# Kernel optimization log

Measured on AMD Instinct MI355X. Metric: run time of the kernel, lower is better.

Reference implementation:

```python
import jax, jax.numpy as jnp
import numpy as np

N_HEADS = 16
ROPE = 64        # qk_rope_head_dim
KV_LORA = 512
V_DIM = 128
THETA = 10000.0

def rms_norm(x, w, eps=1e-6):
    return x * jax.lax.rsqrt(jnp.mean(x * x, axis=-1, keepdims=True) + eps) * w

def rope_cos_sin(T, d, theta=THETA):
    half = d // 2
    inv = 1.0 / theta ** (jnp.arange(half, dtype=jnp.float32) / half)
    ang = jnp.arange(T, dtype=jnp.float32)[:, None] * inv  # (T, half)
    return jnp.cos(ang), jnp.sin(ang)

def apply_rot(x, cos, sin):
    # x: (B,T,H,D); complex rotation on interleaved pairs
    xr, xi = x[..., 0::2], x[..., 1::2]
    c = cos[None, :, None, :]
    s = sin[None, :, None, :]
    orr = xr * c - xi * s
    oi = xr * s + xi * c
    return jnp.stack([orr, oi], axis=-1).reshape(x.shape)

def setup_inputs() -> dict:
    key = jax.random.key(0)
    ks = jax.random.split(key, 8)
    B, T, C = 2, 2048, 2048
    QLR = 1536
    x = jax.random.normal(ks[0], (B, T, C), dtype=jnp.float32)
    mask = jnp.tril(jnp.ones((T, T), dtype=jnp.int32))[None, None]
    sc = 0.02
    w_qa = jax.random.normal(ks[1], (QLR, C), dtype=jnp.float32) * sc
    qa_norm_w = jnp.ones((QLR,), dtype=jnp.float32)
    w_qb = jax.random.normal(ks[2], (N_HEADS * 2 * ROPE, QLR), dtype=jnp.float32) * sc
    w_kva = jax.random.normal(ks[3], (KV_LORA + ROPE, C), dtype=jnp.float32) * sc
    kva_norm_w = jnp.ones((KV_LORA,), dtype=jnp.float32)
    w_kvb = jax.random.normal(ks[4], (N_HEADS * (ROPE + V_DIM), KV_LORA), dtype=jnp.float32) * sc
    w_o = jax.random.normal(ks[5], (C, N_HEADS * V_DIM), dtype=jnp.float32) * sc
    return {"x": x, "mask": mask, "w_qa": w_qa, "qa_norm_w": qa_norm_w, "w_qb": w_qb,
            "w_kva": w_kva, "kva_norm_w": kva_norm_w, "w_kvb": w_kvb, "w_o": w_o}

def reference(x, mask, w_qa, qa_norm_w, w_qb, w_kva, kva_norm_w, w_kvb, w_o):
    B, T, C = x.shape
    # Q: low-rank compress -> norm -> up-project, split nope/rope halves
    q_c = rms_norm(x @ w_qa.T, qa_norm_w)
    q = (q_c @ w_qb.T).reshape(B, T, N_HEADS, 2 * ROPE)
    q_nope, q_rope = q[..., :ROPE], q[..., ROPE:]
    # KV: joint low-rank + shared rope key
    kv_a = x @ w_kva.T
    kv_c = rms_norm(kv_a[..., :KV_LORA], kva_norm_w)
    k_rope_raw = kv_a[..., KV_LORA:]                       # (B,T,ROPE)
    kv = (kv_c @ w_kvb.T).reshape(B, T, N_HEADS, ROPE + V_DIM)
    k_content, v = kv[..., :ROPE], kv[..., ROPE:]
    k_rope = jnp.broadcast_to(k_rope_raw[:, :, None, :], (B, T, N_HEADS, ROPE))
    cos, sin = rope_cos_sin(T, ROPE)
    q_rope = apply_rot(q_rope, cos, sin)
    k_rope = apply_rot(k_rope, cos, sin)
    q = jnp.concatenate([q_nope, q_rope], axis=-1)         # (B,T,H,2*ROPE)
    k = jnp.concatenate([k_content, k_rope], axis=-1)
    att = jnp.einsum('bqhd,bkhd->bhqk', q, k) * (ROPE ** -0.5)
    att = jnp.where(mask == 0, -jnp.inf, att)
    att = jax.nn.softmax(att, axis=-1)
    # source's nan-guard: uniform attention if any nan appeared
    att = jnp.where(jnp.any(jnp.isnan(att)), jnp.float32(1.0 / T), att)
    out = jnp.einsum('bhqk,bkhd->bqhd', att, v).reshape(B, T, N_HEADS * V_DIM)
    return out @ w_o.T
```

## Files before the change

### kernel.cpp

```cpp
#include <hip/hip_runtime.h>

typedef short bf16x8 __attribute__((ext_vector_type(8)));
typedef unsigned short u16x8 __attribute__((ext_vector_type(8)));
typedef unsigned short u16x4 __attribute__((ext_vector_type(4)));
typedef float f32x4 __attribute__((ext_vector_type(4)));
typedef unsigned u32x4 __attribute__((ext_vector_type(4)));
typedef unsigned u32x2 __attribute__((ext_vector_type(2)));

#define DEV static __device__ __forceinline__

DEV float bf2f(unsigned short u) { return __uint_as_float(((unsigned)u) << 16); }
DEV unsigned short f2bf(float f) {
  unsigned u = __float_as_uint(f);
  return (unsigned short)((u + 0x7fffu + ((u >> 16) & 1u)) >> 16);
}
DEV unsigned cvtpk(float lo, float hi) {
  unsigned r;
  asm("v_cvt_pk_bf16_f32 %0, %1, %2" : "=v"(r) : "v"(lo), "v"(hi));
  return r;
}
DEV void p32swap(unsigned& a, unsigned& b) {
  asm volatile("v_permlane32_swap_b32 %0, %1" : "+v"(a), "+v"(b));
}
DEV void p16swap(unsigned& a, unsigned& b) {
  asm volatile("v_permlane16_swap_b32 %0, %1" : "+v"(a), "+v"(b));
}

#define GLDS16(g, l)                                                                   \
  __builtin_amdgcn_global_load_lds((const __attribute__((address_space(1))) void*)(g), \
                                   (__attribute__((address_space(3))) void*)(l), 16, 0, 0)

DEV void cvt_body(const float* __restrict__ src, unsigned short* __restrict__ dst,
                  int rows, int cols, int dstRows, int bid) {
  int i = bid * 256 + (int)threadIdx.x;
  int e = i << 2;
  int r = e / cols;
  int c = e - r * cols;
  u16x4 o = {0, 0, 0, 0};
  if (r < rows) {
    const float* p = src + (size_t)r * cols + c;
    o[0] = f2bf(p[0]); o[1] = f2bf(p[1]); o[2] = f2bf(p[2]); o[3] = f2bf(p[3]);
  }
  *(u16x4*)(dst + e) = o;
}

__global__ __launch_bounds__(256) void convert_all(
    const float* __restrict__ x, const float* __restrict__ w_qa, const float* __restrict__ w_kva,
    const float* __restrict__ w_qb, const float* __restrict__ w_kvb, const float* __restrict__ w_o,
    unsigned short* __restrict__ xb, unsigned short* __restrict__ wqkva,
    unsigned short* __restrict__ wqbb, unsigned short* __restrict__ wkvbb,
    unsigned short* __restrict__ wob) {
  int bid = blockIdx.x;
  if (bid < 8192)        cvt_body(x,     xb,                        4096, 2048, 4096, bid);
  else if (bid < 11264)  cvt_body(w_qa,  wqkva,                     1536, 2048, 1536, bid - 8192);
  else if (bid < 12544)  cvt_body(w_kva, wqkva + (size_t)1536*2048,  576, 2048,  640, bid - 11264);
  else if (bid < 15616)  cvt_body(w_qb,  wqbb,                      2048, 1536, 2048, bid - 12544);
  else if (bid < 17152)  cvt_body(w_kvb, wkvbb,                     3072,  512, 3072, bid - 15616);
  else                   cvt_body(w_o,   wob,                       2048, 2048, 2048, bid - 17152);
}

template <typename OutT>
__global__ __launch_bounds__(256, 2) void gemm_bt(const unsigned short* __restrict__ A,
                                                  const unsigned short* __restrict__ B,
                                                  OutT* __restrict__ C, int M, int N, int K) {
  __shared__ __align__(16) unsigned short As[128 * 64];
  __shared__ __align__(16) unsigned short Bs[128 * 64];
  const int tid = threadIdx.x;
  const int lane = tid & 63, wave = tid >> 6;
  const int l16 = lane & 15, lhi = lane >> 4;
  const int nbn = N >> 7;
  const int bm = blockIdx.x / nbn, bn = blockIdx.x - bm * nbn;
  const int m0 = bm << 7, n0 = bn << 7;
  const int wm = (wave >> 1) << 6, wn = (wave & 1) << 6;
  f32x4 acc[4][4] = {};
  for (int k0 = 0; k0 < K; k0 += 64) {
#pragma unroll
    for (int it = 0; it < 4; ++it) {
      int slot = it * 256 + tid;
      int row = slot >> 3, col = (slot & 7) << 3;
      GLDS16(A + (size_t)(m0 + row) * K + k0 + col, As + (it * 256 + wave * 64) * 8);
      GLDS16(B + (size_t)(n0 + row) * K + k0 + col, Bs + (it * 256 + wave * 64) * 8);
    }
    __syncthreads();
#pragma unroll
    for (int ks = 0; ks < 2; ++ks) {
      bf16x8 a[4], b[4];
#pragma unroll
      for (int i = 0; i < 4; ++i) {
        a[i] = *(const bf16x8*)(As + (wm + i * 16 + l16) * 64 + ks * 32 + lhi * 8);
        b[i] = *(const bf16x8*)(Bs + (wn + i * 16 + l16) * 64 + ks * 32 + lhi * 8);
      }
#pragma unroll
      for (int i = 0; i < 4; ++i)
#pragma unroll
        for (int j = 0; j < 4; ++j)
          acc[i][j] = __builtin_amdgcn_mfma_f32_16x16x32_bf16(a[i], b[j], acc[i][j], 0, 0, 0);
    }
    __syncthreads();
  }
#pragma unroll
  for (int i = 0; i < 4; ++i)
#pragma unroll
    for (int j = 0; j < 4; ++j)
#pragma unroll
      for (int r = 0; r < 4; ++r) {
        int row = m0 + wm + i * 16 + lhi * 4 + r;
        int col = n0 + wn + j * 16 + l16;
        float v = acc[i][j][r];
        if constexpr (sizeof(OutT) == 4)
          C[(size_t)row * N + col] = v;
        else
          C[(size_t)row * N + col] = (OutT)f2bf(v);
      }
}

__global__ __launch_bounds__(256, 2) void gemm_kvb(const unsigned short* __restrict__ A,
                                                   const unsigned short* __restrict__ B,
                                                   unsigned short* __restrict__ kvfull,
                                                   unsigned short* __restrict__ VT) {
  const int M = 4096, N = 3072, K = 512;
  __shared__ __align__(16) unsigned short As[128 * 64];
  __shared__ __align__(16) unsigned short Bs[128 * 64];
  const int tid = threadIdx.x;
  const int lane = tid & 63, wave = tid >> 6;
  const int l16 = lane & 15, lhi = lane >> 4;
  const int nbn = N >> 7;
  const int bm = blockIdx.x / nbn, bn = blockIdx.x - bm * nbn;
  const int m0 = bm << 7, n0 = bn << 7;
  const int wm = (wave >> 1) << 6, wn = (wave & 1) << 6;
  f32x4 acc[4][4] = {};
  for (int k0 = 0; k0 < K; k0 += 64) {
#pragma unroll
    for (int it = 0; it < 4; ++it) {
      int slot = it * 256 + tid;
      int row = slot >> 3, col = (slot & 7) << 3;
      GLDS16(A + (size_t)(m0 + row) * K + k0 + col, As + (it * 256 + wave * 64) * 8);
      GLDS16(B + (size_t)(n0 + row) * K + k0 + col, Bs + (it * 256 + wave * 64) * 8);
    }
    __syncthreads();
#pragma unroll
    for (int ks = 0; ks < 2; ++ks) {
      bf16x8 a[4], b[4];
#pragma unroll
      for (int i = 0; i < 4; ++i) {
        a[i] = *(const bf16x8*)(As + (wm + i * 16 + l16) * 64 + ks * 32 + lhi * 8);
        b[i] = *(const bf16x8*)(Bs + (wn + i * 16 + l16) * 64 + ks * 32 + lhi * 8);
      }
#pragma unroll
      for (int i = 0; i < 4; ++i)
#pragma unroll
        for (int j = 0; j < 4; ++j)
          acc[i][j] = __builtin_amdgcn_mfma_f32_16x16x32_bf16(a[i], b[j], acc[i][j], 0, 0, 0);
    }
    __syncthreads();
  }
#pragma unroll
  for (int i = 0; i < 4; ++i)
#pragma unroll
    for (int j = 0; j < 4; ++j) {
      int col = n0 + wn + j * 16 + l16;
      int h = col / 192;
      int jc = col - h * 192;
      int row0 = m0 + wm + i * 16 + lhi * 4;
      if (jc < 64) {
#pragma unroll
        for (int r = 0; r < 4; ++r)
          kvfull[(size_t)(row0 + r) * 3072 + col] = f2bf(acc[i][j][r]);
      } else {
        int d = jc - 64;
        int b = row0 >> 11, t0 = row0 & 2047;
        u16x4 pk;
#pragma unroll
        for (int r = 0; r < 4; ++r) pk[r] = f2bf(acc[i][j][r]);
        *(u16x4*)(VT + ((size_t)((b * 16 + h) * 128 + d)) * 2048 + t0) = pk;
      }
    }
}

__global__ __launch_bounds__(256) void rms_fused(const unsigned short* __restrict__ qkva,
                                                 const float* __restrict__ qw,
                                                 const float* __restrict__ kvw,
                                                 unsigned short* __restrict__ q_c,
                                                 unsigned short* __restrict__ kv_c,
                                                 unsigned short* __restrict__ krope) {
  const int row = blockIdx.x, tid = threadIdx.x;
  const unsigned short* p = qkva + (size_t)row * 2176;
  float fq[8];
  float ssq = 0.f;
  const bool act = tid < 192;
  if (act) {
    u16x8 v = *(const u16x8*)(p + tid * 8);
#pragma unroll
    for (int j = 0; j < 8; ++j) { fq[j] = bf2f(v[j]); ssq += fq[j] * fq[j]; }
  }
  float f0 = bf2f(p[1536 + tid * 2]), f1 = bf2f(p[1536 + tid * 2 + 1]);
  float sskv = f0 * f0 + f1 * f1;
#pragma unroll
  for (int m = 1; m <= 32; m <<= 1) {
    ssq += __shfl_xor(ssq, m);
    sskv += __shfl_xor(sskv, m);
  }
  __shared__ float rq[4], rkv[4];
  if ((tid & 63) == 0) { rq[tid >> 6] = ssq; rkv[tid >> 6] = sskv; }
  __syncthreads();
  float rstdq = rsqrtf((rq[0] + rq[1] + rq[2] + rq[3]) * (1.f / 1536.f) + 1e-6f);
  float rstdkv = rsqrtf((rkv[0] + rkv[1] + rkv[2] + rkv[3]) * (1.f / 512.f) + 1e-6f);
  if (act) {
    u16x8 o;
#pragma unroll
    for (int j = 0; j < 8; ++j) o[j] = f2bf(fq[j] * rstdq * qw[tid * 8 + j]);
    *(u16x8*)(q_c + (size_t)row * 1536 + tid * 8) = o;
  }
  kv_c[(size_t)row * 512 + tid * 2]     = f2bf(f0 * rstdkv * kvw[tid * 2]);
  kv_c[(size_t)row * 512 + tid * 2 + 1] = f2bf(f1 * rstdkv * kvw[tid * 2 + 1]);
  if (tid < 32) {
    int j = tid;
    float xr = bf2f(p[2048 + 2 * j]), xi = bf2f(p[2048 + 2 * j + 1]);
    int t = row & 2047;
    float ang = (float)t * powf(10000.f, -(float)j * (1.f / 32.f));
    float c = cosf(ang), s = sinf(ang);
    krope[(size_t)row * 64 + 2 * j]     = f2bf(xr * c - xi * s);
    krope[(size_t)row * 64 + 2 * j + 1] = f2bf(xr * s + xi * c);
  }
}

__global__ __launch_bounds__(256, 4) void flash_attn(const unsigned short* __restrict__ qfull,
                                                     const unsigned short* __restrict__ kvfull,
                                                     const unsigned short* __restrict__ krope,
                                                     const unsigned short* __restrict__ Vt,
                                                     unsigned short* __restrict__ out) {
  const int tid = threadIdx.x, lane = tid & 63, wave = tid >> 6;
  const int l16 = lane & 15, lhi = lane >> 4;
  const int bid = blockIdx.x;
  const int xcd = bid & 7, Lb = bid >> 3;
  const int bhl = Lb >> 5, cL = Lb & 31;
  const int s = (bhl & 1) ? (31 - cL) : cL;
  const int bh = xcd * 4 + bhl;
  const int h = bh & 15, b = bh >> 4;
  __shared__ __align__(16) unsigned short Ks[64 * 128];
  __shared__ __align__(16) unsigned short Vs[64 * 128];

  const float QSCALE = 0.125f * 1.44269504089f;
  bf16x8 qf[4];
  f32x4 o_acc[8] = {};
  const int qg = s * 64 + wave * 16 + l16;
  {
    const unsigned short* qrow = qfull + (size_t)(b * 2048 + qg) * 2048 + h * 128;
#pragma unroll
    for (int ks = 0; ks < 4; ++ks) {
      u16x8 raw = *(const u16x8*)(qrow + ks * 32 + lhi * 8);
      float f[8];
#pragma unroll
      for (int j = 0; j < 8; ++j) f[j] = bf2f(raw[j]);
      if (ks >= 2) {
#pragma unroll
        for (int pp = 0; pp < 4; ++pp) {
          int d = ks * 32 + lhi * 8 + 2 * pp;
          int jl = (d - 64) >> 1;
          float ang = (float)qg * powf(10000.f, -(float)jl * (1.f / 32.f));
          float co = cosf(ang), si = sinf(ang);
          float xr = f[2 * pp], xi = f[2 * pp + 1];
          f[2 * pp] = xr * co - xi * si;
          f[2 * pp + 1] = xr * si + xi * co;
        }
      }
      bf16x8 fr;
#pragma unroll
      for (int j = 0; j < 8; ++j) fr[j] = (short)f2bf(f[j] * QSCALE);
      qf[ks] = fr;
    }
  }
  float m_run = -1e30f, l_run = 0.f;

  const int bT = b * 2048;
  const unsigned short* Vbh = Vt + (size_t)(b * 16 + h) * 128 * 2048;

  for (int kt = 0; kt <= s; ++kt) {
#pragma unroll
    for (int it = 0; it < 4; ++it) {
      int Lo = it * 4096 + wave * 1024 + lane * 16;
      int r = Lo >> 8;
      int w = (Lo & 255) ^ ((r & 7) << 4);
      int cc = w >> 1;
      int tl = bT + kt * 64 + r;
      const unsigned short* src = (cc < 64) ? kvfull + (size_t)tl * 3072 + h * 192 + cc
                                            : krope + (size_t)tl * 64 + (cc - 64);
      GLDS16(src, Ks + ((it * 4096 + wave * 1024) >> 1));
    }
#pragma unroll
    for (int it = 0; it < 4; ++it) {
      int Lo = it * 4096 + wave * 1024 + lane * 16;
      int d = Lo >> 7;
      int w = (Lo & 127) ^ ((d & 7) << 4);
      GLDS16(Vbh + (size_t)d * 2048 + kt * 64 + (w >> 1), Vs + ((it * 4096 + wave * 1024) >> 1));
    }
    __syncthreads();

    f32x4 st[4] = {};
    __builtin_amdgcn_s_setprio(1);
#pragma unroll
    for (int ks = 0; ks < 4; ++ks) {
      bf16x8 kf;
#pragma unroll
      for (int nt = 0; nt < 4; ++nt) {
        int row = nt * 16 + l16;
        int byteoff = row * 256 + ((ks * 64 + lhi * 16) ^ ((l16 & 7) << 4));
        kf = *(const bf16x8*)((const char*)Ks + byteoff);
        st[nt] = __builtin_amdgcn_mfma_f32_16x16x32_bf16(kf, qf[ks], st[nt], 0, 0, 0);
      }
    }
    __builtin_amdgcn_s_setprio(0);

    if (kt == s) {
#pragma unroll
      for (int nt = 0; nt < 4; ++nt)
#pragma unroll
        for (int r = 0; r < 4; ++r) {
          int kg = kt * 64 + nt * 16 + lhi * 4 + r;
          st[nt][r] = (kg <= qg) ? st[nt][r] : -1e30f;
        }
    }
    float mx = -1e30f;
#pragma unroll
    for (int nt = 0; nt < 4; ++nt)
#pragma unroll
      for (int r = 0; r < 4; ++r) mx = fmaxf(mx, st[nt][r]);
    mx = fmaxf(mx, __shfl_xor(mx, 16));
    mx = fmaxf(mx, __shfl_xor(mx, 32));
    if (__ballot(mx > m_run + 8.f)) {
      float mnew = fmaxf(m_run, mx);
      float sc = exp2f(m_run - mnew);
      m_run = mnew;
      l_run *= sc;
#pragma unroll
      for (int dt = 0; dt < 8; ++dt) o_acc[dt] *= sc;
    }
    const float mcur = m_run;
    float sum = 0.f;
#pragma unroll
    for (int nt = 0; nt < 4; ++nt)
#pragma unroll
      for (int r = 0; r < 4; ++r) {
        float p = exp2f(st[nt][r] - mcur);
        st[nt][r] = p;
        sum += p;
      }
    sum += __shfl_xor(sum, 16);
    sum += __shfl_xor(sum, 32);
    l_run += sum;
    bf16x8 pw[2];
    {
      unsigned pk01[4], pk23[4];
#pragma unroll
      for (int nt = 0; nt < 4; ++nt) {
        pk01[nt] = cvtpk(st[nt][0], st[nt][1]);
        pk23[nt] = cvtpk(st[nt][2], st[nt][3]);
      }
#pragma unroll
      for (int k2 = 0; k2 < 2; ++k2) {
        unsigned a0 = pk01[2 * k2], b0 = pk01[2 * k2 + 1];
        unsigned a1 = pk23[2 * k2], b1 = pk23[2 * k2 + 1];
        p32swap(a0, b0); p16swap(a0, b0);
        p32swap(a1, b1); p16swap(a1, b1);
        u32x4 t4 = {a0, a1, b0, b1};
        pw[k2] = *(bf16x8*)&t4;
      }
    }

    __builtin_amdgcn_s_setprio(1);
#pragma unroll
    for (int k2 = 0; k2 < 2; ++k2)
#pragma unroll
      for (int dt = 0; dt < 8; ++dt) {
        int row = dt * 16 + l16;
        int byteoff = row * 128 + ((k2 * 64 + lhi * 16) ^ ((l16 & 7) << 4));
        bf16x8 vf = *(const bf16x8*)((const char*)Vs + byteoff);
        o_acc[dt] = __builtin_amdgcn_mfma_f32_16x16x32_bf16(vf, pw[k2], o_acc[dt], 0, 0, 0);
      }
    __builtin_amdgcn_s_setprio(0);

    __syncthreads();
  }

  {
    float inv = 1.0f / l_run;
    unsigned short* orow = out + (size_t)(b * 2048 + qg) * 2048 + h * 128;
#pragma unroll
    for (int dt = 0; dt < 8; ++dt) {
      unsigned w01 = cvtpk(o_acc[dt][0] * inv, o_acc[dt][1] * inv);
      unsigned w23 = cvtpk(o_acc[dt][2] * inv, o_acc[dt][3] * inv);
      u32x2 st2 = {w01, w23};
      *(u32x2*)(orow + dt * 16 + lhi * 4) = st2;
    }
  }
}

extern "C" void kernel_launch(void* const* d_in, const int* in_sizes, int n_in,
                              void* d_out, int out_size, void* d_ws, size_t ws_size,
                              hipStream_t stream) {
  (void)in_sizes; (void)n_in; (void)out_size; (void)ws_size;
  const float* x      = (const float*)d_in[0];
  const float* w_qa   = (const float*)d_in[2];
  const float* qa_nw  = (const float*)d_in[3];
  const float* w_qb   = (const float*)d_in[4];
  const float* w_kva  = (const float*)d_in[5];
  const float* kva_nw = (const float*)d_in[6];
  const float* w_kvb  = (const float*)d_in[7];
  const float* w_o    = (const float*)d_in[8];
  float* out = (float*)d_out;
  char* ws = (char*)d_ws;

  unsigned short* xb     = (unsigned short*)(ws + 0);
  unsigned short* wqkva  = (unsigned short*)(ws + 16777216);
  unsigned short* wqbb   = (unsigned short*)(ws + 25690112);
  unsigned short* wkvbb  = (unsigned short*)(ws + 31981568);
  unsigned short* wob    = (unsigned short*)(ws + 35127296);
  unsigned short* qkva   = (unsigned short*)(ws + 43515904);
  unsigned short* qfull  = (unsigned short*)(ws + 43515904);
  unsigned short* q_c    = (unsigned short*)(ws + 61341696);
  unsigned short* kv_c   = (unsigned short*)(ws + 73924608);
  unsigned short* krope  = (unsigned short*)(ws + 78118912);
  unsigned short* attno  = (unsigned short*)(ws + 61341696);
  unsigned short* Vattn  = (unsigned short*)(ws + 78643200);
  unsigned short* kvfull = (unsigned short*)d_out;

  convert_all<<<21248, 256, 0, stream>>>(x, w_qa, w_kva, w_qb, w_kvb, w_o,
                                         xb, wqkva, wqbb, wkvbb, wob);

  gemm_bt<unsigned short><<<32 * 17, 256, 0, stream>>>(xb, wqkva, qkva, 4096, 2176, 2048);

  rms_fused<<<4096, 256, 0, stream>>>(qkva, qa_nw, kva_nw, q_c, kv_c, krope);

  gemm_bt<unsigned short><<<32 * 16, 256, 0, stream>>>(q_c, wqbb, qfull, 4096, 2048, 1536);
  gemm_kvb<<<32 * 24, 256, 0, stream>>>(kv_c, wkvbb, kvfull, Vattn);

  flash_attn<<<1024, 256, 0, stream>>>(qfull, kvfull, krope, Vattn, attno);

  gemm_bt<float><<<32 * 16, 256, 0, stream>>>(attno, wob, out, 4096, 2048, 2048);
}
```

Baseline: 282.0 us.

## Double-buffer K/V tiles and process two query subtiles per wave in flash attention

Each block now handles 128 query rows (each wave owns two 16-row subtiles), so every K/V tile loaded into shared memory feeds twice as many MFMAs. K/V staging is double-buffered so the next tile's global-to-LDS loads overlap compute on the current one. The grid is halved and blocks are ordered longest-first to balance the causal workload. The cost is higher register and LDS use (launch bounds lowered to 2 blocks per SIMD), which reduces occupancy, and waves whose causal range is shorter sit idle on the last tile.

```diff
diff --git a/kernel.cpp b/kernel.cpp
--- a/kernel.cpp
+++ b/kernel.cpp
@@ -224,7 +224,7 @@
   }
 }
 
-__global__ __launch_bounds__(256, 4) void flash_attn(const unsigned short* __restrict__ qfull,
+__global__ __launch_bounds__(256, 2) void flash_attn(const unsigned short* __restrict__ qfull,
                                                      const unsigned short* __restrict__ kvfull,
                                                      const unsigned short* __restrict__ krope,
                                                      const unsigned short* __restrict__ Vt,
@@ -232,20 +232,24 @@
   const int tid = threadIdx.x, lane = tid & 63, wave = tid >> 6;
   const int l16 = lane & 15, lhi = lane >> 4;
   const int bid = blockIdx.x;
-  const int xcd = bid & 7, Lb = bid >> 3;
-  const int bhl = Lb >> 5, cL = Lb & 31;
-  const int s = (bhl & 1) ? (31 - cL) : cL;
+  const int xcd = bid & 7, idx = bid >> 3;
+  const int s = 15 - (idx >> 2);
+  const int bhl = idx & 3;
   const int bh = xcd * 4 + bhl;
   const int h = bh & 15, b = bh >> 4;
-  __shared__ __align__(16) unsigned short Ks[64 * 128];
-  __shared__ __align__(16) unsigned short Vs[64 * 128];
+  __shared__ __align__(16) unsigned short Ks[2][64 * 128];
+  __shared__ __align__(16) unsigned short Vs[2][64 * 128];
 
   const float QSCALE = 0.125f * 1.44269504089f;
-  bf16x8 qf[4];
-  f32x4 o_acc[8] = {};
-  const int qg = s * 64 + wave * 16 + l16;
-  {
-    const unsigned short* qrow = qfull + (size_t)(b * 2048 + qg) * 2048 + h * 128;
+  bf16x8 qf[2][4];
+  float m_run[2], l_run[2];
+  int qg[2];
+  f32x4 o_acc[2][8] = {};
+#pragma unroll
+  for (int u = 0; u < 2; ++u) {
+    const int t = s * 128 + wave * 32 + u * 16 + l16;
+    qg[u] = t;
+    const unsigned short* qrow = qfull + (size_t)(b * 2048 + t) * 2048 + h * 128;
 #pragma unroll
     for (int ks = 0; ks < 4; ++ks) {
       u16x8 raw = *(const u16x8*)(qrow + ks * 32 + lhi * 8);
@@ -257,7 +261,7 @@
         for (int pp = 0; pp < 4; ++pp) {
           int d = ks * 32 + lhi * 8 + 2 * pp;
           int jl = (d - 64) >> 1;
-          float ang = (float)qg * powf(10000.f, -(float)jl * (1.f / 32.f));
+          float ang = (float)t * powf(10000.f, -(float)jl * (1.f / 32.f));
           float co = cosf(ang), si = sinf(ang);
           float xr = f[2 * pp], xi = f[2 * pp + 1];
           f[2 * pp] = xr * co - xi * si;
@@ -267,15 +271,18 @@
       bf16x8 fr;
 #pragma unroll
       for (int j = 0; j < 8; ++j) fr[j] = (short)f2bf(f[j] * QSCALE);
-      qf[ks] = fr;
-    }
-  }
-  float m_run = -1e30f, l_run = 0.f;
+      qf[u][ks] = fr;
+    }
+    m_run[u] = -1e30f;
+    l_run[u] = 0.f;
+  }
 
   const int bT = b * 2048;
   const unsigned short* Vbh = Vt + (size_t)(b * 16 + h) * 128 * 2048;
-
-  for (int kt = 0; kt <= s; ++kt) {
+  const int ntiles = 2 * s + 2;
+  const int ktmax = 2 * s + (wave >> 1);
+
+  auto stageK = [&](int kt, int buf) {
 #pragma unroll
     for (int it = 0; it < 4; ++it) {
       int Lo = it * 4096 + wave * 1024 + lane * 16;
@@ -285,110 +292,132 @@
       int tl = bT + kt * 64 + r;
       const unsigned short* src = (cc < 64) ? kvfull + (size_t)tl * 3072 + h * 192 + cc
                                             : krope + (size_t)tl * 64 + (cc - 64);
-      GLDS16(src, Ks + ((it * 4096 + wave * 1024) >> 1));
-    }
+      GLDS16(src, &Ks[buf][(it * 4096 + wave * 1024) >> 1]);
+    }
+  };
+  auto stageV = [&](int kt, int buf) {
 #pragma unroll
     for (int it = 0; it < 4; ++it) {
       int Lo = it * 4096 + wave * 1024 + lane * 16;
       int d = Lo >> 7;
       int w = (Lo & 127) ^ ((d & 7) << 4);
-      GLDS16(Vbh + (size_t)d * 2048 + kt * 64 + (w >> 1), Vs + ((it * 4096 + wave * 1024) >> 1));
-    }
+      GLDS16(Vbh + (size_t)d * 2048 + kt * 64 + (w >> 1), &Vs[buf][(it * 4096 + wave * 1024) >> 1]);
+    }
+  };
+
+  stageK(0, 0);
+  stageV(0, 0);
+  __syncthreads();
+  int cur = 0;
+
+  for (int kt = 0; kt < ntiles; ++kt) {
+    if (kt + 1 < ntiles) { stageK(kt + 1, cur ^ 1); stageV(kt + 1, cur ^ 1); }
+    if (kt <= ktmax) {
+      const unsigned short* Kb = Ks[cur];
+      const unsigned short* Vb = Vs[cur];
+
+      f32x4 st[2][4] = {};
+      __builtin_amdgcn_s_setprio(1);
+#pragma unroll
+      for (int ks = 0; ks < 4; ++ks) {
+        bf16x8 kf[4];
+#pragma unroll
+        for (int nt = 0; nt < 4; ++nt) {
+          int row = nt * 16 + l16;
+          int byteoff = row * 256 + ((ks * 64 + lhi * 16) ^ ((l16 & 7) << 4));
+          kf[nt] = *(const bf16x8*)((const char*)Kb + byteoff);
+        }
+#pragma unroll
+        for (int nt = 0; nt < 4; ++nt) {
+          st[0][nt] = __builtin_amdgcn_mfma_f32_16x16x32_bf16(kf[nt], qf[0][ks], st[0][nt], 0, 0, 0);
+          st[1][nt] = __builtin_amdgcn_mfma_f32_16x16x32_bf16(kf[nt], qf[1][ks], st[1][nt], 0, 0, 0);
+        }
+      }
+      __builtin_amdgcn_s_setprio(0);
+
+      bf16x8 pw[2][2];
+#pragma unroll
+      for (int u = 0; u < 2; ++u) {
+        if (kt == ktmax) {
+#pragma unroll
+          for (int nt = 0; nt < 4; ++nt)
+#pragma unroll
+            for (int r = 0; r < 4; ++r) {
+              int kg = kt * 64 + nt * 16 + lhi * 4 + r;
+              st[u][nt][r] = (kg <= qg[u]) ? st[u][nt][r] : -1e30f;
+            }
+        }
+        float mx = -1e30f;
+#pragma unroll
+        for (int nt = 0; nt < 4; ++nt)
+#pragma unroll
+          for (int r = 0; r < 4; ++r) mx = fmaxf(mx, st[u][nt][r]);
+        mx = fmaxf(mx, __shfl_xor(mx, 16));
+        mx = fmaxf(mx, __shfl_xor(mx, 32));
+        if (__ballot(mx > m_run[u] + 8.f)) {
+          float mnew = fmaxf(m_run[u], mx);
+          float sc = exp2f(m_run[u] - mnew);
+          m_run[u] = mnew;
+          l_run[u] *= sc;
+#pragma unroll
+          for (int dt = 0; dt < 8; ++dt) o_acc[u][dt] *= sc;
+        }
+        const float mcur = m_run[u];
+        float sum = 0.f;
+#pragma unroll
+        for (int nt = 0; nt < 4; ++nt)
+#pragma unroll
+          for (int r = 0; r < 4; ++r) {
+            float p = exp2f(st[u][nt][r] - mcur);
+            st[u][nt][r] = p;
+            sum += p;
+          }
+        sum += __shfl_xor(sum, 16);
+        sum += __shfl_xor(sum, 32);
+        l_run[u] += sum;
+        unsigned pk01[4], pk23[4];
+#pragma unroll
+        for (int nt = 0; nt < 4; ++nt) {
+          pk01[nt] = cvtpk(st[u][nt][0], st[u][nt][1]);
+          pk23[nt] = cvtpk(st[u][nt][2], st[u][nt][3]);
+        }
+#pragma unroll
+        for (int k2 = 0; k2 < 2; ++k2) {
+          unsigned a0 = pk01[2 * k2], b0 = pk01[2 * k2 + 1];
+          unsigned a1 = pk23[2 * k2], b1 = pk23[2 * k2 + 1];
+          p32swap(a0, b0); p16swap(a0, b0);
+          p32swap(a1, b1); p16swap(a1, b1);
+          u32x4 t4 = {a0, a1, b0, b1};
+          pw[u][k2] = *(bf16x8*)&t4;
+        }
+      }
+
+      __builtin_amdgcn_s_setprio(1);
+#pragma unroll
+      for (int k2 = 0; k2 < 2; ++k2)
+#pragma unroll
+        for (int dt = 0; dt < 8; ++dt) {
+          int row = dt * 16 + l16;
+          int byteoff = row * 128 + ((k2 * 64 + lhi * 16) ^ ((l16 & 7) << 4));
+          bf16x8 vf = *(const bf16x8*)((const char*)Vb + byteoff);
+          o_acc[0][dt] = __builtin_amdgcn_mfma_f32_16x16x32_bf16(vf, pw[0][k2], o_acc[0][dt], 0, 0, 0);
+          o_acc[1][dt] = __builtin_amdgcn_mfma_f32_16x16x32_bf16(vf, pw[1][k2], o_acc[1][dt], 0, 0, 0);
+        }
+      __builtin_amdgcn_s_setprio(0);
+    }
+
     __syncthreads();
-
-    f32x4 st[4] = {};
-    __builtin_amdgcn_s_setprio(1);
-#pragma unroll
-    for (int ks = 0; ks < 4; ++ks) {
-      bf16x8 kf;
-#pragma unroll
-      for (int nt = 0; nt < 4; ++nt) {
-        int row = nt * 16 + l16;
-        int byteoff = row * 256 + ((ks * 64 + lhi * 16) ^ ((l16 & 7) << 4));
-        kf = *(const bf16x8*)((const char*)Ks + byteoff);
-        st[nt] = __builtin_amdgcn_mfma_f32_16x16x32_bf16(kf, qf[ks], st[nt], 0, 0, 0);
-      }
-    }
-    __builtin_amdgcn_s_setprio(0);
-
-    if (kt == s) {
-#pragma unroll
-      for (int nt = 0; nt < 4; ++nt)
-#pragma unroll
-        for (int r = 0; r < 4; ++r) {
-          int kg = kt * 64 + nt * 16 + lhi * 4 + r;
-          st[nt][r] = (kg <= qg) ? st[nt][r] : -1e30f;
-        }
-    }
-    float mx = -1e30f;
-#pragma unroll
-    for (int nt = 0; nt < 4; ++nt)
-#pragma unroll
-      for (int r = 0; r < 4; ++r) mx = fmaxf(mx, st[nt][r]);
-    mx = fmaxf(mx, __shfl_xor(mx, 16));
-    mx = fmaxf(mx, __shfl_xor(mx, 32));
-    if (__ballot(mx > m_run + 8.f)) {
-      float mnew = fmaxf(m_run, mx);
-      float sc = exp2f(m_run - mnew);
-      m_run = mnew;
-      l_run *= sc;
-#pragma unroll
-      for (int dt = 0; dt < 8; ++dt) o_acc[dt] *= sc;
-    }
-    const float mcur = m_run;
-    float sum = 0.f;
-#pragma unroll
-    for (int nt = 0; nt < 4; ++nt)
-#pragma unroll
-      for (int r = 0; r < 4; ++r) {
-        float p = exp2f(st[nt][r] - mcur);
-        st[nt][r] = p;
-        sum += p;
-      }
-    sum += __shfl_xor(sum, 16);
-    sum += __shfl_xor(sum, 32);
-    l_run += sum;
-    bf16x8 pw[2];
-    {
-      unsigned pk01[4], pk23[4];
-#pragma unroll
-      for (int nt = 0; nt < 4; ++nt) {
-        pk01[nt] = cvtpk(st[nt][0], st[nt][1]);
-        pk23[nt] = cvtpk(st[nt][2], st[nt][3]);
-      }
-#pragma unroll
-      for (int k2 = 0; k2 < 2; ++k2) {
-        unsigned a0 = pk01[2 * k2], b0 = pk01[2 * k2 + 1];
-        unsigned a1 = pk23[2 * k2], b1 = pk23[2 * k2 + 1];
-        p32swap(a0, b0); p16swap(a0, b0);
-        p32swap(a1, b1); p16swap(a1, b1);
-        u32x4 t4 = {a0, a1, b0, b1};
-        pw[k2] = *(bf16x8*)&t4;
-      }
-    }
-
-    __builtin_amdgcn_s_setprio(1);
-#pragma unroll
-    for (int k2 = 0; k2 < 2; ++k2)
-#pragma unroll
-      for (int dt = 0; dt < 8; ++dt) {
-        int row = dt * 16 + l16;
-        int byteoff = row * 128 + ((k2 * 64 + lhi * 16) ^ ((l16 & 7) << 4));
-        bf16x8 vf = *(const bf16x8*)((const char*)Vs + byteoff);
-        o_acc[dt] = __builtin_amdgcn_mfma_f32_16x16x32_bf16(vf, pw[k2], o_acc[dt], 0, 0, 0);
-      }
-    __builtin_amdgcn_s_setprio(0);
-
-    __syncthreads();
-  }
-
-  {
-    float inv = 1.0f / l_run;
-    unsigned short* orow = out + (size_t)(b * 2048 + qg) * 2048 + h * 128;
+    cur ^= 1;
+  }
+
+#pragma unroll
+  for (int u = 0; u < 2; ++u) {
+    float inv = 1.0f / l_run[u];
+    unsigned short* orow = out + (size_t)(b * 2048 + qg[u]) * 2048 + h * 128;
 #pragma unroll
     for (int dt = 0; dt < 8; ++dt) {
-      unsigned w01 = cvtpk(o_acc[dt][0] * inv, o_acc[dt][1] * inv);
-      unsigned w23 = cvtpk(o_acc[dt][2] * inv, o_acc[dt][3] * inv);
+      unsigned w01 = cvtpk(o_acc[u][dt][0] * inv, o_acc[u][dt][1] * inv);
+      unsigned w23 = cvtpk(o_acc[u][dt][2] * inv, o_acc[u][dt][3] * inv);
       u32x2 st2 = {w01, w23};
       *(u32x2*)(orow + dt * 16 + lhi * 4) = st2;
     }
@@ -434,7 +463,7 @@
   gemm_bt<unsigned short><<<32 * 16, 256, 0, stream>>>(q_c, wqbb, qfull, 4096, 2048, 1536);
   gemm_kvb<<<32 * 24, 256, 0, stream>>>(kv_c, wkvbb, kvfull, Vattn);
 
-  flash_attn<<<1024, 256, 0, stream>>>(qfull, kvfull, krope, Vattn, attno);
+  flash_attn<<<512, 256, 0, stream>>>(qfull, kvfull, krope, Vattn, attno);
 
   gemm_bt<float><<<32 * 16, 256, 0, stream>>>(attno, wob, out, 4096, 2048, 2048);
 }
```

Result: slower. 287.9 us (+2.1%).

## Prefetch next K/V tile into registers while computing current tile

Applied to the files above, without the earlier changes.

Replaces direct global-to-LDS loads with register staging: the next K and V tiles are loaded into registers at the start of each iteration, overlapping with the QK and PV MFMA work, then written to LDS after the compute barrier. This aims to hide global load latency behind compute. In exchange it adds 32 VGPRs of staging, an extra barrier per iteration, and explicit LDS stores. Register pressure could lower occupancy under the 4-blocks launch bound.

```diff
diff --git a/kernel.cpp b/kernel.cpp
--- a/kernel.cpp
+++ b/kernel.cpp
@@ -238,7 +238,7 @@
   const int bh = xcd * 4 + bhl;
   const int h = bh & 15, b = bh >> 4;
   __shared__ __align__(16) unsigned short Ks[64 * 128];
-  __shared__ __align__(16) unsigned short Vs[64 * 128];
+  __shared__ __align__(16) unsigned short Vs[128 * 64];
 
   const float QSCALE = 0.125f * 1.44269504089f;
   bf16x8 qf[4];
@@ -275,7 +275,9 @@
   const int bT = b * 2048;
   const unsigned short* Vbh = Vt + (size_t)(b * 16 + h) * 128 * 2048;
 
-  for (int kt = 0; kt <= s; ++kt) {
+  u32x4 kr0, kr1, kr2, kr3, vr0, vr1, vr2, vr3;
+  auto loadK = [&](int kt, u32x4& d0, u32x4& d1, u32x4& d2, u32x4& d3) {
+    u32x4* dsts[4] = {&d0, &d1, &d2, &d3};
 #pragma unroll
     for (int it = 0; it < 4; ++it) {
       int Lo = it * 4096 + wave * 1024 + lane * 16;
@@ -285,27 +287,50 @@
       int tl = bT + kt * 64 + r;
       const unsigned short* src = (cc < 64) ? kvfull + (size_t)tl * 3072 + h * 192 + cc
                                             : krope + (size_t)tl * 64 + (cc - 64);
-      GLDS16(src, Ks + ((it * 4096 + wave * 1024) >> 1));
-    }
+      *dsts[it] = *(const u32x4*)src;
+    }
+  };
+  auto loadV = [&](int kt, u32x4& d0, u32x4& d1, u32x4& d2, u32x4& d3) {
+    u32x4* dsts[4] = {&d0, &d1, &d2, &d3};
 #pragma unroll
     for (int it = 0; it < 4; ++it) {
       int Lo = it * 4096 + wave * 1024 + lane * 16;
       int d = Lo >> 7;
       int w = (Lo & 127) ^ ((d & 7) << 4);
-      GLDS16(Vbh + (size_t)d * 2048 + kt * 64 + (w >> 1), Vs + ((it * 4096 + wave * 1024) >> 1));
-    }
-    __syncthreads();
+      *dsts[it] = *(const u32x4*)(Vbh + (size_t)d * 2048 + kt * 64 + (w >> 1));
+    }
+  };
+  auto writeKV = [&]() {
+#pragma unroll
+    for (int it = 0; it < 4; ++it) {
+      int off = it * 4096 + wave * 1024 + lane * 16;
+      u32x4 kv_ = (it == 0) ? kr0 : (it == 1) ? kr1 : (it == 2) ? kr2 : kr3;
+      u32x4 vv_ = (it == 0) ? vr0 : (it == 1) ? vr1 : (it == 2) ? vr2 : vr3;
+      *(u32x4*)((char*)Ks + off) = kv_;
+      *(u32x4*)((char*)Vs + off) = vv_;
+    }
+  };
+
+  loadK(0, kr0, kr1, kr2, kr3);
+  loadV(0, vr0, vr1, vr2, vr3);
+  writeKV();
+  __syncthreads();
+
+  for (int kt = 0; kt <= s; ++kt) {
+    if (kt < s) {
+      loadK(kt + 1, kr0, kr1, kr2, kr3);
+      loadV(kt + 1, vr0, vr1, vr2, vr3);
+    }
 
     f32x4 st[4] = {};
     __builtin_amdgcn_s_setprio(1);
 #pragma unroll
     for (int ks = 0; ks < 4; ++ks) {
-      bf16x8 kf;
 #pragma unroll
       for (int nt = 0; nt < 4; ++nt) {
         int row = nt * 16 + l16;
         int byteoff = row * 256 + ((ks * 64 + lhi * 16) ^ ((l16 & 7) << 4));
-        kf = *(const bf16x8*)((const char*)Ks + byteoff);
+        bf16x8 kf = *(const bf16x8*)((const char*)Ks + byteoff);
         st[nt] = __builtin_amdgcn_mfma_f32_16x16x32_bf16(kf, qf[ks], st[nt], 0, 0, 0);
       }
     }
@@ -380,6 +405,10 @@
     __builtin_amdgcn_s_setprio(0);
 
     __syncthreads();
+    if (kt < s) {
+      writeKV();
+      __syncthreads();
+    }
   }
 
   {
```

Result: slower. 356.3 us (+26.3%).
